# Performance work log

Hardware: AMD Instinct MI355X
Metric: run time of the kernel (lower is better)

Reference implementation:

```python
import jax, jax.numpy as jnp
import numpy as np


def setup_inputs() -> dict:
    key = jax.random.key(0)
    kx, kwl, kbl, kwr = jax.random.split(key, 4)
    B = 64          # batch of identical DAGs
    L = 11          # number of levels (leaves = level 0)
    NPL = 10000     # nodes per level
    K = 16          # children per non-leaf node
    N = L * NPL     # 110000 nodes per graph
    # Build a layered DAG: edges go child (level l-1) -> father (level l),
    # matching the module's convention edge_index[0]=child, edge_index[1]=father
    # (leaves are nodes with in-degree 0).
    rng = np.random.default_rng(0)
    srcs, dsts = [], []
    for l in range(1, L):
        fathers = np.arange(l * NPL, (l + 1) * NPL)
        children = rng.integers((l - 1) * NPL, l * NPL, size=(NPL, K))
        srcs.append(children.reshape(-1))
        dsts.append(np.repeat(fathers, K))
    edge_index = jnp.asarray(
        np.stack([np.concatenate(srcs), np.concatenate(dsts)]), dtype=jnp.int32
    )  # [2, E] with E = (L-1)*NPL*K = 1.6M
    x = jax.random.normal(kx, (B, N, 1), dtype=jnp.float32)
    w_l = jax.random.normal(kwl, (1, 1), dtype=jnp.float32)   # lin_l weight (1->1)
    b_l = jax.random.normal(kbl, (1,), dtype=jnp.float32) * 0.1  # lin_l bias
    w_r = jax.random.normal(kwr, (1, 1), dtype=jnp.float32)   # lin_r weight (no bias)
    return {"x": x, "w_l": w_l, "b_l": b_l, "w_r": w_r,
            "edge_index": edge_index, "num_levels": L - 1}


def _dagprop(x, w_l, b_l, w_r, edge_index, num_levels):
    # x: [B, N, 1] scalar node features for B identical DAGs.
    src, dst = edge_index[0], edge_index[1]
    N = x.shape[1]
    xb = x[..., 0]  # [B, N]
    indeg = jnp.zeros((N,), jnp.int32).at[dst].add(1)  # in-degree (children count)
    is_leaf = indeg == 0
    # Init: out[leaves] = tanh(x[leaves]); out[non-leaves] = lin_r(x) (no bias).
    out = jnp.where(is_leaf[None, :], jnp.tanh(xb), xb * w_r[0, 0])  # [B, N]
    visited = is_leaf
    inv_deg = 1.0 / jnp.maximum(indeg, 1).astype(xb.dtype)
    for _ in range(num_levels):
        # fathers whose children are ALL visited become the next frontier
        nvis = jnp.zeros((N,), jnp.int32).at[dst].add(visited[src].astype(jnp.int32))
        ready = (~visited) & (indeg > 0) & (nvis == indeg)
        # scatter-mean of children's outputs over all incoming edges (aggr='mean');
        # only consumed at 'ready' nodes, whose children are all visited.
        agg = jnp.zeros_like(out).at[:, dst].add(out[:, src]) * inv_deg[None, :]
        # out[next] = tanh(out[next] + lin_l(agg[next]))
        new = jnp.tanh(out + agg * w_l[0, 0] + b_l[0])
        out = jnp.where(ready[None, :], new, out)
        visited = visited | ready
    return out[..., None]  # [B, N, 1]


def reference(x, w_l, b_l, w_r, edge_index, num_levels):
    return _dagprop(x, w_l, b_l, w_r, edge_index, num_levels)
```

## Files before the change

### kernel.cpp

```cpp
#include <hip/hip_runtime.h>
#include <math.h>

#define BATCH   64
#define NPL     10000
#define NLEV    10
#define NNODE   110000
#define KCH     16
#define SLICES  4
#define FPB     (NPL / SLICES)
#define THREADS 1024
#define NBLOCKS (BATCH * SLICES)

#define FR_F    10240
#define FR_F4   2560
#define SL_F4   625
#define FOREIGN_F4 (3 * SL_F4)
#define EXCH_FLOATS (2 * BATCH * FR_F)
#define ALLSET  0x01010101u

__device__ inline void coh_store(float* p, float v) {
    __hip_atomic_store(p, v, __ATOMIC_RELAXED, __HIP_MEMORY_SCOPE_AGENT);
}
__device__ inline void flag_set(unsigned char* p) {
    __hip_atomic_store(p, (unsigned char)1, __ATOMIC_RELAXED,
                       __HIP_MEMORY_SCOPE_AGENT);
}
__device__ inline unsigned int flag_poll(const unsigned int* p) {
    return __hip_atomic_load(p, __ATOMIC_RELAXED, __HIP_MEMORY_SCOPE_AGENT);
}

__device__ inline void coh_load4_x2(const float4* p0, const float4* p1,
                                    float4& a, float4& b) {
    asm volatile("global_load_dwordx4 %0, %2, off sc0 sc1\n\t"
                 "global_load_dwordx4 %1, %3, off sc0 sc1\n\t"
                 "s_waitcnt vmcnt(0)"
                 : "=&v"(a), "=&v"(b)
                 : "v"(p0), "v"(p1)
                 : "memory");
}

#define GATHER16(BUF, c0, c1, c2, c3, off)                                  \
    (BUF[c0.x - off] + BUF[c0.y - off] + BUF[c0.z - off] + BUF[c0.w - off]  \
   + BUF[c1.x - off] + BUF[c1.y - off] + BUF[c1.z - off] + BUF[c1.w - off]  \
   + BUF[c2.x - off] + BUF[c2.y - off] + BUF[c2.z - off] + BUF[c2.w - off]  \
   + BUF[c3.x - off] + BUF[c3.y - off] + BUF[c3.z - off] + BUF[c3.w - off])

__global__ __launch_bounds__(THREADS, 4) void k_dag_s4(
    const float* __restrict__ x,
    float*       __restrict__ out,
    const int4*  __restrict__ src4,
    float*       __restrict__ exch,
    unsigned int* __restrict__ flags,
    const float* __restrict__ wl_p,
    const float* __restrict__ bl_p,
    const float* __restrict__ wr_p)
{
    __shared__ float buf[2][FR_F];
    const int blk = blockIdx.x;
    const int b   = blk >> 2;
    const int q   = blk & 3;
    const int tid = threadIdx.x;
    const float wr   = wr_p[0];
    const float wl16 = wl_p[0] * (1.0f / 16.0f);
    const float bl   = bl_p[0];
    const float* __restrict__ xb = x   + (size_t)b * NNODE;
    float*       __restrict__ ob = out + (size_t)b * NNODE;
    const int f0 = q * FPB;
    unsigned int* myflag = flags + b * 16;

    const int j1  = tid;
    const int a1  = j1 + ((j1 >= q * SL_F4) ? SL_F4 : 0);
    const int j2  = tid + 1024;
    const int j2e = (j2 < FOREIGN_F4) ? j2 : (FOREIGN_F4 - 1);
    const int a2  = j2e + ((j2e >= q * SL_F4) ? SL_F4 : 0);

    {
        float* ex0 = exch + (size_t)b * FR_F;
        const int i1 = f0 + tid, i2 = i1 + 1024, i3 = i1 + 2048;
        float v1 = tanhf(xb[i1]); ob[i1] = v1; coh_store(ex0 + i1, v1); buf[0][i1] = v1;
        float v2 = tanhf(xb[i2]); ob[i2] = v2; coh_store(ex0 + i2, v2); buf[0][i2] = v2;
        if (tid < FPB - 2048) {
            float v3 = tanhf(xb[i3]); ob[i3] = v3; coh_store(ex0 + i3, v3); buf[0][i3] = v3;
        }
    }
    __syncthreads();
    if (tid == 0) flag_set((unsigned char*)(myflag + 0) + q);

    for (int l = 1; l <= NLEV; ++l) {
        const int pprev = (l - 1) & 1;
        const int off   = (l - 1) * NPL;
        const int nodeb = l * NPL;
        const int4* sp  = src4 + (size_t)((l - 1) * NPL) * (KCH / 4);

        const int fA = f0 + tid, fB = fA + 1024;
        const int4 pa0 = sp[fA*4+0], pa1 = sp[fA*4+1], pa2 = sp[fA*4+2], pa3 = sp[fA*4+3];
        const int4 pb0 = sp[fB*4+0], pb1 = sp[fB*4+1], pb2 = sp[fB*4+2], pb3 = sp[fB*4+3];
        const float xA = xb[nodeb + fA];
        const float xB = xb[nodeb + fB];

        if (tid == 0)
            while (flag_poll(myflag + (l - 1)) != ALLSET) __builtin_amdgcn_s_sleep(1);
        asm volatile("" ::: "memory");
        __syncthreads();

        const int t3 = tid + 2048;
        const int fC = f0 + ((t3 < FPB) ? t3 : (FPB - 1));
        const int4 pc0 = sp[fC*4+0], pc1 = sp[fC*4+1], pc2 = sp[fC*4+2], pc3 = sp[fC*4+3];
        const float xC = xb[nodeb + fC];

        {
            const float4* exr = (const float4*)(exch + ((size_t)pprev * BATCH + b) * FR_F);
            float4 r1, r2;
            coh_load4_x2(exr + a1, exr + a2, r1, r2);
            float4* bufv = (float4*)buf[pprev];
            bufv[a1] = r1;
            bufv[a2] = r2;
        }
        __syncthreads();

        const float* __restrict__ prevb = buf[pprev];
        float* __restrict__ nextb = buf[l & 1];
        float* exw = exch + ((size_t)(l & 1) * BATCH + b) * FR_F;
        {
            float s = GATHER16(prevb, pa0, pa1, pa2, pa3, off);
            float v = tanhf(fmaf(s, wl16, fmaf(xA, wr, bl)));
            ob[nodeb + fA] = v;
            if (l < NLEV) { coh_store(exw + fA, v); nextb[fA] = v; }
        }
        {
            float s = GATHER16(prevb, pb0, pb1, pb2, pb3, off);
            float v = tanhf(fmaf(s, wl16, fmaf(xB, wr, bl)));
            ob[nodeb + fB] = v;
            if (l < NLEV) { coh_store(exw + fB, v); nextb[fB] = v; }
        }
        if (t3 < FPB) {
            float s = GATHER16(prevb, pc0, pc1, pc2, pc3, off);
            float v = tanhf(fmaf(s, wl16, fmaf(xC, wr, bl)));
            ob[nodeb + fC] = v;
            if (l < NLEV) { coh_store(exw + fC, v); nextb[fC] = v; }
        }

        if (l < NLEV) {
            __syncthreads();
            if (tid == 0) flag_set((unsigned char*)(myflag + l) + q);
        }
    }
}

extern "C" void kernel_launch(void* const* d_in, const int* in_sizes, int n_in,
                              void* d_out, int out_size, void* d_ws, size_t ws_size,
                              hipStream_t stream) {
    const float* x  = (const float*)d_in[0];
    const float* wl = (const float*)d_in[1];
    const float* bl = (const float*)d_in[2];
    const float* wr = (const float*)d_in[3];
    const int*   ei = (const int*)d_in[4];

    const int4* src4 = (const int4*)ei;
    float* out  = (float*)d_out;
    float* exch = (float*)d_ws;
    unsigned int* flags = (unsigned int*)((char*)d_ws + (size_t)EXCH_FLOATS * sizeof(float));

    (void)hipMemsetAsync(flags, 0, BATCH * 16 * sizeof(unsigned int), stream);
    k_dag_s4<<<NBLOCKS, THREADS, 0, stream>>>(
        x, out, src4, exch, flags, wl, bl, wr);
}
```

Measured before the change: 157.2 us.

## Split each DAG across eight 512-thread blocks with single LDS buffer

Each batch graph is now partitioned across 8 cooperating blocks of 512 threads instead of 4 blocks of 1024, so more CUs work on each level and per-block critical paths are shorter. The level-ready flags widen to 64-bit words so all 8 slice bytes can be polled at once, and each block's foreign-slice fetch grows to five float4 loads per thread. The double-buffered LDS frontier is replaced by one buffer, with each block's own values refilled from registers after the barrier. The trade-off is more cross-block exchange traffic and more producers per flag, and the spin-wait still requires all 512 blocks to be co-resident.

```diff
diff --git a/kernel.cpp b/kernel.cpp
--- a/kernel.cpp
+++ b/kernel.cpp
@@ -6,17 +6,17 @@
 #define NLEV    10
 #define NNODE   110000
 #define KCH     16
-#define SLICES  4
-#define FPB     (NPL / SLICES)
-#define THREADS 1024
+#define SLICES  8
+#define FPB     1280
+#define THREADS 512
 #define NBLOCKS (BATCH * SLICES)
 
 #define FR_F    10240
 #define FR_F4   2560
-#define SL_F4   625
-#define FOREIGN_F4 (3 * SL_F4)
+#define SL_F4   320
+#define FOREIGN_F4 (7 * SL_F4)
 #define EXCH_FLOATS (2 * BATCH * FR_F)
-#define ALLSET  0x01010101u
+#define ALL8    0x0101010101010101ULL
 
 __device__ inline void coh_store(float* p, float v) {
     __hip_atomic_store(p, v, __ATOMIC_RELAXED, __HIP_MEMORY_SCOPE_AGENT);
@@ -25,17 +25,23 @@
     __hip_atomic_store(p, (unsigned char)1, __ATOMIC_RELAXED,
                        __HIP_MEMORY_SCOPE_AGENT);
 }
-__device__ inline unsigned int flag_poll(const unsigned int* p) {
+__device__ inline unsigned long long flag_poll(const unsigned long long* p) {
     return __hip_atomic_load(p, __ATOMIC_RELAXED, __HIP_MEMORY_SCOPE_AGENT);
 }
 
-__device__ inline void coh_load4_x2(const float4* p0, const float4* p1,
-                                    float4& a, float4& b) {
-    asm volatile("global_load_dwordx4 %0, %2, off sc0 sc1\n\t"
-                 "global_load_dwordx4 %1, %3, off sc0 sc1\n\t"
+__device__ inline void coh_load4_x5(const float4* p0, const float4* p1,
+                                    const float4* p2, const float4* p3,
+                                    const float4* p4,
+                                    float4& a, float4& b, float4& c,
+                                    float4& d, float4& e) {
+    asm volatile("global_load_dwordx4 %0, %5, off sc0 sc1\n\t"
+                 "global_load_dwordx4 %1, %6, off sc0 sc1\n\t"
+                 "global_load_dwordx4 %2, %7, off sc0 sc1\n\t"
+                 "global_load_dwordx4 %3, %8, off sc0 sc1\n\t"
+                 "global_load_dwordx4 %4, %9, off sc0 sc1\n\t"
                  "s_waitcnt vmcnt(0)"
-                 : "=&v"(a), "=&v"(b)
-                 : "v"(p0), "v"(p1)
+                 : "=&v"(a), "=&v"(b), "=&v"(c), "=&v"(d), "=&v"(e)
+                 : "v"(p0), "v"(p1), "v"(p2), "v"(p3), "v"(p4)
                  : "memory");
 }
 
@@ -45,43 +51,48 @@
    + BUF[c2.x - off] + BUF[c2.y - off] + BUF[c2.z - off] + BUF[c2.w - off]  \
    + BUF[c3.x - off] + BUF[c3.y - off] + BUF[c3.z - off] + BUF[c3.w - off])
 
-__global__ __launch_bounds__(THREADS, 4) void k_dag_s4(
+__global__ __launch_bounds__(THREADS, 4) void k_dag_sb(
     const float* __restrict__ x,
     float*       __restrict__ out,
     const int4*  __restrict__ src4,
     float*       __restrict__ exch,
-    unsigned int* __restrict__ flags,
+    unsigned long long* __restrict__ flags,
     const float* __restrict__ wl_p,
     const float* __restrict__ bl_p,
     const float* __restrict__ wr_p)
 {
-    __shared__ float buf[2][FR_F];
+    __shared__ float buf[FR_F];
     const int blk = blockIdx.x;
-    const int b   = blk >> 2;
-    const int q   = blk & 3;
+    const int b   = blk >> 3;
+    const int q   = blk & 7;
     const int tid = threadIdx.x;
     const float wr   = wr_p[0];
     const float wl16 = wl_p[0] * (1.0f / 16.0f);
     const float bl   = bl_p[0];
     const float* __restrict__ xb = x   + (size_t)b * NNODE;
     float*       __restrict__ ob = out + (size_t)b * NNODE;
-    const int f0 = q * FPB;
-    unsigned int* myflag = flags + b * 16;
+    const int f0    = q * FPB;
+    const int fpb_q = (NPL - f0 < FPB) ? (NPL - f0) : FPB;
+    unsigned long long* myflag = flags + b * 16;
 
-    const int j1  = tid;
-    const int a1  = j1 + ((j1 >= q * SL_F4) ? SL_F4 : 0);
-    const int j2  = tid + 1024;
-    const int j2e = (j2 < FOREIGN_F4) ? j2 : (FOREIGN_F4 - 1);
-    const int a2  = j2e + ((j2e >= q * SL_F4) ? SL_F4 : 0);
+    int am[5];
+#pragma unroll
+    for (int it = 0; it < 5; ++it) {
+        int j  = tid + it * THREADS;
+        int je = (j < FOREIGN_F4) ? j : (FOREIGN_F4 - 1);
+        am[it] = je + ((je >= q * SL_F4) ? SL_F4 : 0);
+    }
+
+    const bool has1 = (tid + THREADS)     < fpb_q;
+    const bool has2 = (tid + 2 * THREADS) < fpb_q;
+    float v0, v1 = 0.f, v2 = 0.f;
 
     {
         float* ex0 = exch + (size_t)b * FR_F;
-        const int i1 = f0 + tid, i2 = i1 + 1024, i3 = i1 + 2048;
-        float v1 = tanhf(xb[i1]); ob[i1] = v1; coh_store(ex0 + i1, v1); buf[0][i1] = v1;
-        float v2 = tanhf(xb[i2]); ob[i2] = v2; coh_store(ex0 + i2, v2); buf[0][i2] = v2;
-        if (tid < FPB - 2048) {
-            float v3 = tanhf(xb[i3]); ob[i3] = v3; coh_store(ex0 + i3, v3); buf[0][i3] = v3;
-        }
+        const int i0 = f0 + tid;
+        v0 = tanhf(xb[i0]); ob[i0] = v0; coh_store(ex0 + i0, v0);
+        if (has1) { v1 = tanhf(xb[i0 + 512]);  ob[i0 + 512]  = v1; coh_store(ex0 + i0 + 512,  v1); }
+        if (has2) { v2 = tanhf(xb[i0 + 1024]); ob[i0 + 1024] = v2; coh_store(ex0 + i0 + 1024, v2); }
     }
     __syncthreads();
     if (tid == 0) flag_set((unsigned char*)(myflag + 0) + q);
@@ -90,54 +101,56 @@
         const int pprev = (l - 1) & 1;
         const int off   = (l - 1) * NPL;
         const int nodeb = l * NPL;
-        const int4* sp  = src4 + (size_t)((l - 1) * NPL) * (KCH / 4);
+        const int4* sp  = src4 + (size_t)off * (KCH / 4);
 
-        const int fA = f0 + tid, fB = fA + 1024;
+        const int fA = f0 + tid, fB = fA + THREADS;
         const int4 pa0 = sp[fA*4+0], pa1 = sp[fA*4+1], pa2 = sp[fA*4+2], pa3 = sp[fA*4+3];
         const int4 pb0 = sp[fB*4+0], pb1 = sp[fB*4+1], pb2 = sp[fB*4+2], pb3 = sp[fB*4+3];
         const float xA = xb[nodeb + fA];
         const float xB = xb[nodeb + fB];
 
         if (tid == 0)
-            while (flag_poll(myflag + (l - 1)) != ALLSET) __builtin_amdgcn_s_sleep(1);
+            while (flag_poll(myflag + (l - 1)) != ALL8) __builtin_amdgcn_s_sleep(1);
         asm volatile("" ::: "memory");
         __syncthreads();
 
-        const int t3 = tid + 2048;
-        const int fC = f0 + ((t3 < FPB) ? t3 : (FPB - 1));
+        const int fCr = f0 + tid + 2 * THREADS;
+        const int fC  = (fCr < f0 + fpb_q) ? fCr : (f0 + fpb_q - 1);
         const int4 pc0 = sp[fC*4+0], pc1 = sp[fC*4+1], pc2 = sp[fC*4+2], pc3 = sp[fC*4+3];
         const float xC = xb[nodeb + fC];
 
         {
+            buf[f0 + tid] = v0;
+            if (has1) buf[f0 + tid + 512]  = v1;
+            if (has2) buf[f0 + tid + 1024] = v2;
             const float4* exr = (const float4*)(exch + ((size_t)pprev * BATCH + b) * FR_F);
-            float4 r1, r2;
-            coh_load4_x2(exr + a1, exr + a2, r1, r2);
-            float4* bufv = (float4*)buf[pprev];
-            bufv[a1] = r1;
-            bufv[a2] = r2;
+            float4 r0, r1, r2, r3, r4;
+            coh_load4_x5(exr + am[0], exr + am[1], exr + am[2], exr + am[3], exr + am[4],
+                         r0, r1, r2, r3, r4);
+            float4* bufv = (float4*)buf;
+            bufv[am[0]] = r0; bufv[am[1]] = r1; bufv[am[2]] = r2;
+            bufv[am[3]] = r3; bufv[am[4]] = r4;
         }
         __syncthreads();
 
-        const float* __restrict__ prevb = buf[pprev];
-        float* __restrict__ nextb = buf[l & 1];
         float* exw = exch + ((size_t)(l & 1) * BATCH + b) * FR_F;
         {
-            float s = GATHER16(prevb, pa0, pa1, pa2, pa3, off);
-            float v = tanhf(fmaf(s, wl16, fmaf(xA, wr, bl)));
-            ob[nodeb + fA] = v;
-            if (l < NLEV) { coh_store(exw + fA, v); nextb[fA] = v; }
+            float s = GATHER16(buf, pa0, pa1, pa2, pa3, off);
+            v0 = tanhf(fmaf(s, wl16, fmaf(xA, wr, bl)));
+            ob[nodeb + fA] = v0;
+            if (l < NLEV) coh_store(exw + fA, v0);
         }
-        {
-            float s = GATHER16(prevb, pb0, pb1, pb2, pb3, off);
-            float v = tanhf(fmaf(s, wl16, fmaf(xB, wr, bl)));
-            ob[nodeb + fB] = v;
-            if (l < NLEV) { coh_store(exw + fB, v); nextb[fB] = v; }
+        if (has1) {
+            float s = GATHER16(buf, pb0, pb1, pb2, pb3, off);
+            v1 = tanhf(fmaf(s, wl16, fmaf(xB, wr, bl)));
+            ob[nodeb + fB] = v1;
+            if (l < NLEV) coh_store(exw + fB, v1);
         }
-        if (t3 < FPB) {
-            float s = GATHER16(prevb, pc0, pc1, pc2, pc3, off);
-            float v = tanhf(fmaf(s, wl16, fmaf(xC, wr, bl)));
-            ob[nodeb + fC] = v;
-            if (l < NLEV) { coh_store(exw + fC, v); nextb[fC] = v; }
+        if (has2) {
+            float s = GATHER16(buf, pc0, pc1, pc2, pc3, off);
+            v2 = tanhf(fmaf(s, wl16, fmaf(xC, wr, bl)));
+            ob[nodeb + fC] = v2;
+            if (l < NLEV) coh_store(exw + fC, v2);
         }
 
         if (l < NLEV) {
@@ -159,9 +172,10 @@
     const int4* src4 = (const int4*)ei;
     float* out  = (float*)d_out;
     float* exch = (float*)d_ws;
-    unsigned int* flags = (unsigned int*)((char*)d_ws + (size_t)EXCH_FLOATS * sizeof(float));
+    unsigned long long* flags =
+        (unsigned long long*)((char*)d_ws + (size_t)EXCH_FLOATS * sizeof(float));
 
-    (void)hipMemsetAsync(flags, 0, BATCH * 16 * sizeof(unsigned int), stream);
-    k_dag_s4<<<NBLOCKS, THREADS, 0, stream>>>(
+    (void)hipMemsetAsync(flags, 0, BATCH * 16 * sizeof(unsigned long long), stream);
+    k_dag_sb<<<NBLOCKS, THREADS, 0, stream>>>(
         x, out, src4, exch, flags, wl, bl, wr);
 }
```

After: 145.6 us. 7.4% less time.
